# Performance work log

Hardware: AMD Instinct MI355X
Metric: run time of the kernel (lower is better)

The kernel has to match this reference:

```python
import jax, jax.numpy as jnp
import numpy as np

INPUT_SIZE = 512
HIDDEN_SIZE = 512
BATCH = 64
SEQ = 1024

def _xavier(key, shape):
    fan_in, fan_out = shape
    limit = float(np.sqrt(6.0 / (fan_in + fan_out)))
    return jax.random.uniform(key, shape, jnp.float32, -limit, limit)

def setup_inputs() -> dict:
    key = jax.random.key(0)
    ks = jax.random.split(key, 9)
    x = jax.random.normal(ks[0], (BATCH, SEQ, INPUT_SIZE), jnp.float32)
    # Concatenate the 4 input-hidden and 4 hidden-hidden weights (i,f,g,o order)
    W_i = jnp.concatenate([_xavier(ks[1 + j], (INPUT_SIZE, HIDDEN_SIZE)) for j in range(4)], axis=1)  # [I, 4H]
    W_h = jnp.concatenate([_xavier(ks[5 + j], (HIDDEN_SIZE, HIDDEN_SIZE)) for j in range(4)], axis=1)  # [H, 4H]
    b = jnp.zeros((4 * HIDDEN_SIZE,), jnp.float32)  # b_ii+b_hi etc. are both zero-init; combined bias
    return {"x": x, "W_i": W_i, "W_h": W_h, "b": b}

def reference(x, W_i, W_h, b):
    H = W_h.shape[0]
    B = x.shape[0]
    # Precompute all input projections in one big GEMM: [B, S, 4H]
    x_proj = jnp.einsum('bsi,ig->bsg', x, W_i) + b

    def step(carry, xp_t):
        h, c = carry
        gates = xp_t + h @ W_h  # [B, 4H]
        i_t = jax.nn.sigmoid(gates[:, 0*H:1*H])
        f_t = jax.nn.sigmoid(gates[:, 1*H:2*H])
        g_t = jnp.tanh(gates[:, 2*H:3*H])
        o_t = jax.nn.sigmoid(gates[:, 3*H:4*H])
        c = f_t * c + i_t * g_t
        h = o_t * jnp.tanh(c)
        return (h, c), None

    h0 = jnp.zeros((B, H), x.dtype)
    c0 = jnp.zeros((B, H), x.dtype)
    (h_t, c_t), _ = jax.lax.scan(step, (h0, c0), jnp.swapaxes(x_proj, 0, 1))
    return (h_t, c_t)
```

## Files before the change

### kernel.cpp

```cpp
#include <hip/hip_runtime.h>
#include <hip/hip_bf16.h>
#include <hip/hip_cooperative_groups.h>

namespace cg = cooperative_groups;

typedef unsigned short ushort_t;
typedef unsigned int uint32;
typedef __attribute__((ext_vector_type(8))) __bf16 bf16x8;
typedef __attribute__((ext_vector_type(4))) float f32x4;
typedef __attribute__((ext_vector_type(4))) unsigned int u32x4;

#define SEQ_LEN 1024
#define NWG 64
#define NTHR 256

#define XPACK_BYTES (64ull << 20)
#define WPACK_BYTES (4ull << 20)
#define HB_OFF  (XPACK_BYTES + WPACK_BYTES)
#define CNT_OFF (HB_OFF + (128ull << 10))
#define WS_NEED (CNT_OFF + (64ull << 10))

__device__ __forceinline__ ushort_t f2bf(float f) {
  unsigned u = __builtin_bit_cast(unsigned, f);
  unsigned r = (u + 0x7fffu + ((u >> 16) & 1u)) >> 16;
  return (ushort_t)r;
}
__device__ __forceinline__ float sigm(float x) {
  float e = __expf(-x);
  return __builtin_amdgcn_rcpf(1.f + e);
}
__device__ __forceinline__ float tanh_fast(float x) {
  float a = fabsf(x);
  float e = __expf(-2.f * a);
  float r = (1.f - e) * __builtin_amdgcn_rcpf(1.f + e);
  return copysignf(r, x);
}

__global__ void zero_mem_kernel(u32x4* p) {
  int i = blockIdx.x * blockDim.x + threadIdx.x;
  u32x4 z = {0u, 0u, 0u, 0u};
  p[i] = z;
}

__global__ void pack_x_kernel(const float* __restrict__ x, u32x4* __restrict__ xp) {
  unsigned u = blockIdx.x * blockDim.x + threadIdx.x;
  int hi = u & 3;
  int kk = (u >> 2) & 15;
  int t  = (u >> 6) & 1023;
  int b  = u >> 16;
  const float* src = x + (((size_t)b * SEQ_LEN + t) * 512 + (kk << 5) + (hi << 3));
  f32x4 f0 = *(const f32x4*)(src);
  f32x4 f1 = *(const f32x4*)(src + 4);
  u32x4 o;
  o[0] = f2bf(f0[0]) | ((uint32)f2bf(f0[1]) << 16);
  o[1] = f2bf(f0[2]) | ((uint32)f2bf(f0[3]) << 16);
  o[2] = f2bf(f1[0]) | ((uint32)f2bf(f1[1]) << 16);
  o[3] = f2bf(f1[2]) | ((uint32)f2bf(f1[3]) << 16);
  xp[(size_t)((t * 16 + kk) * 64 + b) * 4 + hi] = o;
}

__global__ void pack_w_kernel(const float* __restrict__ Wi, const float* __restrict__ Wh,
                              ushort_t* __restrict__ wp) {
  unsigned e = blockIdx.x * blockDim.x + threadIdx.x;
  int k = e >> 11;
  int col = e & 2047;
  float v = (k < 512) ? Wi[(size_t)k * 2048 + col] : Wh[(size_t)(k - 512) * 2048 + col];
  int wg  = (col & 511) >> 3;
  int tau = (col >> 2) & 1;
  int hcl = col & 3;
  int gate = col >> 9;
  int p = (hcl << 2) | gate;
  int kk = k >> 5;
  int hi = (k >> 3) & 3;
  int r = k & 7;
  int lane = (hi << 4) | p;
  wp[(size_t)wg * 32768 + (size_t)(((kk * 2) + tau) * 64 + lane) * 8 + r] = f2bf(v);
}

template<bool FAST>
__global__ void __launch_bounds__(NTHR, 1)
lstm_coop(const float* __restrict__ x, const float* __restrict__ Wi,
          const float* __restrict__ Wh, const float* __restrict__ bias,
          const u32x4* __restrict__ xpack, const u32x4* __restrict__ wpack,
          ushort_t* hbuf, uint32* flags, float* out)
{
  __shared__ u32x4 lA[4096];
  const int tid  = threadIdx.x;
  const int wg   = blockIdx.x;
  const int lane = tid & 63;
  const int wv   = tid >> 6;
  const int hi2  = lane >> 4;
  const int lo   = lane & 15;
  const int b    = (wv << 4) | lo;

  if (FAST) {
    const u32x4* wsrc = wpack + (size_t)wg * 2048 * 2;
    for (int i = tid; i < 4096; i += NTHR) lA[i] = wsrc[i];
  } else {
    for (int uu = tid; uu < 4096; uu += NTHR) {
      int ln = uu & 63, tau = (uu >> 6) & 1, kk = uu >> 7;
      int uhi = ln >> 4, p = ln & 15;
      int gate = p & 3, hcl = p >> 2;
      int col = gate * 512 + (wg << 3) + tau * 4 + hcl;
      ushort_t tmp[8];
#pragma unroll
      for (int r = 0; r < 8; ++r) {
        int k = (kk << 5) + (uhi << 3) + r;
        float f = (k < 512) ? Wi[(size_t)k * 2048 + col] : Wh[(size_t)(k - 512) * 2048 + col];
        tmp[r] = f2bf(f);
      }
      u32x4 v;
      v[0] = tmp[0] | ((uint32)tmp[1] << 16);
      v[1] = tmp[2] | ((uint32)tmp[3] << 16);
      v[2] = tmp[4] | ((uint32)tmp[5] << 16);
      v[3] = tmp[6] | ((uint32)tmp[7] << 16);
      lA[uu] = v;
    }
  }
  __syncthreads();

  const int kh0 = (wg << 3) | hi2;
  const int kh1 = kh0 + 4;
  const float b00 = bias[0 * 512 + kh0], b01 = bias[1 * 512 + kh0];
  const float b02 = bias[2 * 512 + kh0], b03 = bias[3 * 512 + kh0];
  const float b10 = bias[0 * 512 + kh1], b11 = bias[1 * 512 + kh1];
  const float b12 = bias[2 * 512 + kh1], b13 = bias[3 * 512 + kh1];

  const int hoff0 = (((kh0 >> 5) * 256 + b * 4 + ((kh0 >> 3) & 3)) << 3) + (kh0 & 7);
  const int hoff1 = hoff0 + 4;

  bf16x8 whA[16], whB[16];
#pragma unroll
  for (int kk = 0; kk < 16; ++kk) {
    whA[kk] = __builtin_bit_cast(bf16x8, lA[((16 + kk) * 2 + 0) * 64 + lane]);
    whB[kk] = __builtin_bit_cast(bf16x8, lA[((16 + kk) * 2 + 1) * 64 + lane]);
  }

  float c0 = 0.f, c1 = 0.f, hn0 = 0.f, hn1 = 0.f;
  cg::grid_group grid = cg::this_grid();

  for (int t = 0; t < SEQ_LEN; ++t) {
    f32x4 ax0 = {b00, b01, b02, b03};
    f32x4 ax1 = {b10, b11, b12, b13};
    if (FAST) {
      const u32x4* xb = xpack + (size_t)t * 4096 + b * 4 + hi2;
#pragma unroll
      for (int kk = 0; kk < 16; ++kk) {
        bf16x8 xv = __builtin_bit_cast(bf16x8, xb[kk * 256]);
        bf16x8 a0 = __builtin_bit_cast(bf16x8, lA[(kk * 2 + 0) * 64 + lane]);
        bf16x8 a1 = __builtin_bit_cast(bf16x8, lA[(kk * 2 + 1) * 64 + lane]);
        ax0 = __builtin_amdgcn_mfma_f32_16x16x32_bf16(a0, xv, ax0, 0, 0, 0);
        ax1 = __builtin_amdgcn_mfma_f32_16x16x32_bf16(a1, xv, ax1, 0, 0, 0);
      }
    } else {
      const float* xr = x + ((size_t)b * SEQ_LEN + t) * 512 + (hi2 << 3);
#pragma unroll
      for (int kk = 0; kk < 16; ++kk) {
        f32x4 f0 = *(const f32x4*)(xr + (kk << 5));
        f32x4 f1 = *(const f32x4*)(xr + (kk << 5) + 4);
        u32x4 v;
        v[0] = f2bf(f0[0]) | ((uint32)f2bf(f0[1]) << 16);
        v[1] = f2bf(f0[2]) | ((uint32)f2bf(f0[3]) << 16);
        v[2] = f2bf(f1[0]) | ((uint32)f2bf(f1[1]) << 16);
        v[3] = f2bf(f1[2]) | ((uint32)f2bf(f1[3]) << 16);
        bf16x8 xv = __builtin_bit_cast(bf16x8, v);
        bf16x8 a0 = __builtin_bit_cast(bf16x8, lA[(kk * 2 + 0) * 64 + lane]);
        bf16x8 a1 = __builtin_bit_cast(bf16x8, lA[(kk * 2 + 1) * 64 + lane]);
        ax0 = __builtin_amdgcn_mfma_f32_16x16x32_bf16(a0, xv, ax0, 0, 0, 0);
        ax1 = __builtin_amdgcn_mfma_f32_16x16x32_bf16(a1, xv, ax1, 0, 0, 0);
      }
    }

    if (FAST) {
      if (t > 0) {
        const u32x4* fa = (const u32x4*)flags + lane;
        const uint32 tt = (uint32)t;
        while (true) {
          u32x4 v;
          asm volatile("global_load_dwordx4 %0, %1, off sc0 sc1\n\ts_waitcnt vmcnt(0)"
                       : "=v"(v) : "v"(fa) : "memory");
          bool ok = (v[0] >= tt) & (v[1] >= tt) & (v[2] >= tt) & (v[3] >= tt);
          if (__all(ok)) break;
        }
      }
    }

    const u32x4* hr = (const u32x4*)hbuf + (size_t)(t & 1) * 4096 + b * 4 + hi2;
    u32x4 hreg[16];
    if (FAST) {
#pragma unroll
      for (int kk = 0; kk < 16; ++kk)
        asm volatile("global_load_dwordx4 %0, %1, off sc0 sc1"
                     : "=v"(hreg[kk]) : "v"(hr + kk * 256) : "memory");
      asm volatile("s_waitcnt vmcnt(0)" ::: "memory");
      __builtin_amdgcn_sched_barrier(0);
    } else {
#pragma unroll
      for (int kk = 0; kk < 16; ++kk) hreg[kk] = hr[kk * 256];
    }

    f32x4 ah0 = {0.f, 0.f, 0.f, 0.f};
    f32x4 ah1 = {0.f, 0.f, 0.f, 0.f};
#pragma unroll
    for (int kk = 0; kk < 16; ++kk) {
      bf16x8 hv = __builtin_bit_cast(bf16x8, hreg[kk]);
      ah0 = __builtin_amdgcn_mfma_f32_16x16x32_bf16(whA[kk], hv, ah0, 0, 0, 0);
      ah1 = __builtin_amdgcn_mfma_f32_16x16x32_bf16(whB[kk], hv, ah1, 0, 0, 0);
    }

    {
      float gi = ax0[0] + ah0[0], gf = ax0[1] + ah0[1];
      float gg = ax0[2] + ah0[2], go = ax0[3] + ah0[3];
      float it = sigm(gi), ft = sigm(gf), ot = sigm(go), gt = tanh_fast(gg);
      c0 = ft * c0 + it * gt;
      hn0 = ot * tanh_fast(c0);
    }
    {
      float gi = ax1[0] + ah1[0], gf = ax1[1] + ah1[1];
      float gg = ax1[2] + ah1[2], go = ax1[3] + ah1[3];
      float it = sigm(gi), ft = sigm(gf), ot = sigm(go), gt = tanh_fast(gg);
      c1 = ft * c1 + it * gt;
      hn1 = ot * tanh_fast(c1);
    }

    if (t < SEQ_LEN - 1) {
      ushort_t* hw = hbuf + (size_t)((t + 1) & 1) * 32768;
      if (FAST) {
        uint32 v0 = f2bf(hn0), v1 = f2bf(hn1);
        asm volatile("global_store_short %0, %1, off sc0 sc1"
                     :: "v"(hw + hoff0), "v"(v0) : "memory");
        asm volatile("global_store_short %0, %1, off sc0 sc1"
                     :: "v"(hw + hoff1), "v"(v1) : "memory");
        asm volatile("s_waitcnt vmcnt(0)" ::: "memory");
        __builtin_amdgcn_sched_barrier(0);
        if (lane == 0) {
          uint32* fp = flags + (wg << 2) + wv;
          uint32 val = (uint32)(t + 1);
          asm volatile("global_store_dword %0, %1, off sc0 sc1"
                       :: "v"(fp), "v"(val) : "memory");
        }
      } else {
        hw[hoff0] = f2bf(hn0);
        hw[hoff1] = f2bf(hn1);
        __threadfence();
        grid.sync();
        __threadfence();
      }
    } else if (!FAST) {
      __threadfence();
      grid.sync();
    }
  }

  out[(size_t)b * 512 + kh0] = hn0;
  out[(size_t)b * 512 + kh1] = hn1;
  out[32768 + (size_t)b * 512 + kh0] = c0;
  out[32768 + (size_t)b * 512 + kh1] = c1;
}

extern "C" void kernel_launch(void* const* d_in, const int* in_sizes, int n_in,
                              void* d_out, int out_size, void* d_ws, size_t ws_size,
                              hipStream_t stream) {
  const float* x    = (const float*)d_in[0];
  const float* Wi   = (const float*)d_in[1];
  const float* Wh   = (const float*)d_in[2];
  const float* bias = (const float*)d_in[3];
  float* out = (float*)d_out;

  bool fast = (d_ws != nullptr) && (ws_size >= WS_NEED);

  if (fast) {
    const u32x4* xpack = (const u32x4*)d_ws;
    const u32x4* wpack = (const u32x4*)((char*)d_ws + XPACK_BYTES);
    ushort_t* hbuf = (ushort_t*)((char*)d_ws + HB_OFF);
    uint32* flags = (uint32*)((char*)d_ws + CNT_OFF);

    zero_mem_kernel<<<48, 256, 0, stream>>>((u32x4*)((char*)d_ws + HB_OFF));
    pack_x_kernel<<<16384, 256, 0, stream>>>(x, (u32x4*)d_ws);
    pack_w_kernel<<<8192, 256, 0, stream>>>(Wi, Wh, (ushort_t*)((char*)d_ws + XPACK_BYTES));

    void* args[] = {(void*)&x, (void*)&Wi, (void*)&Wh, (void*)&bias,
                    (void*)&xpack, (void*)&wpack, (void*)&hbuf, (void*)&flags, (void*)&out};
    void (*kfn)(const float*, const float*, const float*, const float*,
                const u32x4*, const u32x4*, ushort_t*, uint32*, float*) = lstm_coop<true>;
    hipLaunchCooperativeKernel(reinterpret_cast<void*>(kfn), dim3(NWG), dim3(NTHR),
                               args, 0, stream);
  } else {
    ushort_t* hbuf = (ushort_t*)d_out;
    uint32* flags = (uint32*)d_out;
    const u32x4* xpack = (const u32x4*)x;
    const u32x4* wpack = (const u32x4*)Wi;

    zero_mem_kernel<<<16, 256, 0, stream>>>((u32x4*)d_out);

    void* args[] = {(void*)&x, (void*)&Wi, (void*)&Wh, (void*)&bias,
                    (void*)&xpack, (void*)&wpack, (void*)&hbuf, (void*)&flags, (void*)&out};
    void (*kfn)(const float*, const float*, const float*, const float*,
                const u32x4*, const u32x4*, ushort_t*, uint32*, float*) = lstm_coop<false>;
    hipLaunchCooperativeKernel(reinterpret_cast<void*>(kfn), dim3(NWG), dim3(NTHR),
                               args, 0, stream);
  }
}
```

Before: 3.231 ms.

## Tag hidden-state words with timestep to replace flag polling with data polling

Each bf16 hidden value is now stored as a 32-bit word whose high half carries the timestep, so consumers poll the hidden-state buffer itself and proceed once every loaded word has the expected tag. This removes the separate flag array, the store-wait before publishing a flag, and the extra round trip of flag-then-data loads on each step. In exchange every step loads twice as many bytes of hidden state and repacks them before the MFMAs. The fast path also switches from a cooperative launch to a normal launch, which relies on all 64 workgroups being co-resident.

```diff
diff --git a/kernel.cpp b/kernel.cpp
--- a/kernel.cpp
+++ b/kernel.cpp
@@ -17,8 +17,7 @@
 #define XPACK_BYTES (64ull << 20)
 #define WPACK_BYTES (4ull << 20)
 #define HB_OFF  (XPACK_BYTES + WPACK_BYTES)
-#define CNT_OFF (HB_OFF + (128ull << 10))
-#define WS_NEED (CNT_OFF + (64ull << 10))
+#define WS_NEED (HB_OFF + (256ull << 10))
 
 __device__ __forceinline__ ushort_t f2bf(float f) {
   unsigned u = __builtin_bit_cast(unsigned, f);
@@ -35,6 +34,7 @@
   float r = (1.f - e) * __builtin_amdgcn_rcpf(1.f + e);
   return copysignf(r, x);
 }
+__device__ __forceinline__ uint32 umin2(uint32 a, uint32 b) { return a < b ? a : b; }
 
 __global__ void zero_mem_kernel(u32x4* p) {
   int i = blockIdx.x * blockDim.x + threadIdx.x;
@@ -82,7 +82,7 @@
 lstm_coop(const float* __restrict__ x, const float* __restrict__ Wi,
           const float* __restrict__ Wh, const float* __restrict__ bias,
           const u32x4* __restrict__ xpack, const u32x4* __restrict__ wpack,
-          ushort_t* hbuf, uint32* flags, float* out)
+          uint32* hbuf32, ushort_t* hbuf16, float* out)
 {
   __shared__ u32x4 lA[4096];
   const int tid  = threadIdx.x;
@@ -93,7 +93,7 @@
   const int lo   = lane & 15;
   const int b    = (wv << 4) | lo;
 
-  if (FAST) {
+  if constexpr (FAST) {
     const u32x4* wsrc = wpack + (size_t)wg * 2048 * 2;
     for (int i = tid; i < 4096; i += NTHR) lA[i] = wsrc[i];
   } else {
@@ -137,12 +137,11 @@
   }
 
   float c0 = 0.f, c1 = 0.f, hn0 = 0.f, hn1 = 0.f;
-  cg::grid_group grid = cg::this_grid();
 
   for (int t = 0; t < SEQ_LEN; ++t) {
     f32x4 ax0 = {b00, b01, b02, b03};
     f32x4 ax1 = {b10, b11, b12, b13};
-    if (FAST) {
+    if constexpr (FAST) {
       const u32x4* xb = xpack + (size_t)t * 4096 + b * 4 + hi2;
 #pragma unroll
       for (int kk = 0; kk < 16; ++kk) {
@@ -171,41 +170,52 @@
       }
     }
 
-    if (FAST) {
-      if (t > 0) {
-        const u32x4* fa = (const u32x4*)flags + lane;
-        const uint32 tt = (uint32)t;
-        while (true) {
-          u32x4 v;
-          asm volatile("global_load_dwordx4 %0, %1, off sc0 sc1\n\ts_waitcnt vmcnt(0)"
-                       : "=v"(v) : "v"(fa) : "memory");
-          bool ok = (v[0] >= tt) & (v[1] >= tt) & (v[2] >= tt) & (v[3] >= tt);
-          if (__all(ok)) break;
-        }
-      }
-    }
-
-    const u32x4* hr = (const u32x4*)hbuf + (size_t)(t & 1) * 4096 + b * 4 + hi2;
-    u32x4 hreg[16];
-    if (FAST) {
-#pragma unroll
-      for (int kk = 0; kk < 16; ++kk)
-        asm volatile("global_load_dwordx4 %0, %1, off sc0 sc1"
-                     : "=v"(hreg[kk]) : "v"(hr + kk * 256) : "memory");
-      asm volatile("s_waitcnt vmcnt(0)" ::: "memory");
-      __builtin_amdgcn_sched_barrier(0);
-    } else {
-#pragma unroll
-      for (int kk = 0; kk < 16; ++kk) hreg[kk] = hr[kk * 256];
-    }
-
     f32x4 ah0 = {0.f, 0.f, 0.f, 0.f};
     f32x4 ah1 = {0.f, 0.f, 0.f, 0.f};
-#pragma unroll
-    for (int kk = 0; kk < 16; ++kk) {
-      bf16x8 hv = __builtin_bit_cast(bf16x8, hreg[kk]);
-      ah0 = __builtin_amdgcn_mfma_f32_16x16x32_bf16(whA[kk], hv, ah0, 0, 0, 0);
-      ah1 = __builtin_amdgcn_mfma_f32_16x16x32_bf16(whB[kk], hv, ah1, 0, 0, 0);
+
+    if constexpr (FAST) {
+      const u32x4* hr = (const u32x4*)hbuf32 + (size_t)(t & 1) * 8192
+                        + ((size_t)b * 4 + hi2) * 2;
+      const uint32 thr = (uint32)t << 16;
+      u32x4 hreg[32];
+      while (true) {
+#pragma unroll
+        for (int kk = 0; kk < 16; ++kk) {
+          asm volatile("global_load_dwordx4 %0, %1, off sc0 sc1"
+                       : "=v"(hreg[2 * kk]) : "v"(hr + kk * 512) : "memory");
+          asm volatile("global_load_dwordx4 %0, %1, off sc0 sc1"
+                       : "=v"(hreg[2 * kk + 1]) : "v"(hr + kk * 512 + 1) : "memory");
+        }
+        asm volatile("s_waitcnt vmcnt(0)" ::: "memory");
+        __builtin_amdgcn_sched_barrier(0);
+        uint32 mn = 0xFFFFFFFFu;
+#pragma unroll
+        for (int i = 0; i < 32; ++i) {
+          u32x4 v = hreg[i];
+          mn = umin2(mn, umin2(umin2(v[0], v[1]), umin2(v[2], v[3])));
+        }
+        if (__all(mn >= thr)) break;
+      }
+#pragma unroll
+      for (int kk = 0; kk < 16; ++kk) {
+        u32x4 lo4 = hreg[2 * kk], hi4 = hreg[2 * kk + 1];
+        u32x4 p;
+        p[0] = (lo4[0] & 0xFFFFu) | (lo4[1] << 16);
+        p[1] = (lo4[2] & 0xFFFFu) | (lo4[3] << 16);
+        p[2] = (hi4[0] & 0xFFFFu) | (hi4[1] << 16);
+        p[3] = (hi4[2] & 0xFFFFu) | (hi4[3] << 16);
+        bf16x8 hv = __builtin_bit_cast(bf16x8, p);
+        ah0 = __builtin_amdgcn_mfma_f32_16x16x32_bf16(whA[kk], hv, ah0, 0, 0, 0);
+        ah1 = __builtin_amdgcn_mfma_f32_16x16x32_bf16(whB[kk], hv, ah1, 0, 0, 0);
+      }
+    } else {
+      const u32x4* hr = (const u32x4*)hbuf16 + (size_t)(t & 1) * 4096 + b * 4 + hi2;
+#pragma unroll
+      for (int kk = 0; kk < 16; ++kk) {
+        bf16x8 hv = __builtin_bit_cast(bf16x8, hr[kk * 256]);
+        ah0 = __builtin_amdgcn_mfma_f32_16x16x32_bf16(whA[kk], hv, ah0, 0, 0, 0);
+        ah1 = __builtin_amdgcn_mfma_f32_16x16x32_bf16(whB[kk], hv, ah1, 0, 0, 0);
+      }
     }
 
     {
@@ -224,31 +234,28 @@
     }
 
     if (t < SEQ_LEN - 1) {
-      ushort_t* hw = hbuf + (size_t)((t + 1) & 1) * 32768;
-      if (FAST) {
-        uint32 v0 = f2bf(hn0), v1 = f2bf(hn1);
-        asm volatile("global_store_short %0, %1, off sc0 sc1"
-                     :: "v"(hw + hoff0), "v"(v0) : "memory");
-        asm volatile("global_store_short %0, %1, off sc0 sc1"
-                     :: "v"(hw + hoff1), "v"(v1) : "memory");
-        asm volatile("s_waitcnt vmcnt(0)" ::: "memory");
-        __builtin_amdgcn_sched_barrier(0);
-        if (lane == 0) {
-          uint32* fp = flags + (wg << 2) + wv;
-          uint32 val = (uint32)(t + 1);
-          asm volatile("global_store_dword %0, %1, off sc0 sc1"
-                       :: "v"(fp), "v"(val) : "memory");
-        }
+      if constexpr (FAST) {
+        uint32* hw = hbuf32 + (size_t)((t + 1) & 1) * 32768;
+        uint32 tag = (uint32)(t + 1) << 16;
+        uint32 w0 = tag | f2bf(hn0);
+        uint32 w1 = tag | f2bf(hn1);
+        asm volatile("global_store_dword %0, %1, off sc0 sc1"
+                     :: "v"(hw + hoff0), "v"(w0) : "memory");
+        asm volatile("global_store_dword %0, %1, off sc0 sc1"
+                     :: "v"(hw + hoff1), "v"(w1) : "memory");
       } else {
+        ushort_t* hw = hbuf16 + (size_t)((t + 1) & 1) * 32768;
         hw[hoff0] = f2bf(hn0);
         hw[hoff1] = f2bf(hn1);
         __threadfence();
-        grid.sync();
+        cg::this_grid().sync();
         __threadfence();
       }
-    } else if (!FAST) {
-      __threadfence();
-      grid.sync();
+    } else {
+      if constexpr (!FAST) {
+        __threadfence();
+        cg::this_grid().sync();
+      }
     }
   }
 
@@ -272,31 +279,27 @@
   if (fast) {
     const u32x4* xpack = (const u32x4*)d_ws;
     const u32x4* wpack = (const u32x4*)((char*)d_ws + XPACK_BYTES);
-    ushort_t* hbuf = (ushort_t*)((char*)d_ws + HB_OFF);
-    uint32* flags = (uint32*)((char*)d_ws + CNT_OFF);
-
-    zero_mem_kernel<<<48, 256, 0, stream>>>((u32x4*)((char*)d_ws + HB_OFF));
+    uint32* hbuf32 = (uint32*)((char*)d_ws + HB_OFF);
+    ushort_t* hbuf16 = (ushort_t*)d_out;
+
+    zero_mem_kernel<<<64, 256, 0, stream>>>((u32x4*)((char*)d_ws + HB_OFF));
     pack_x_kernel<<<16384, 256, 0, stream>>>(x, (u32x4*)d_ws);
     pack_w_kernel<<<8192, 256, 0, stream>>>(Wi, Wh, (ushort_t*)((char*)d_ws + XPACK_BYTES));
 
-    void* args[] = {(void*)&x, (void*)&Wi, (void*)&Wh, (void*)&bias,
-                    (void*)&xpack, (void*)&wpack, (void*)&hbuf, (void*)&flags, (void*)&out};
-    void (*kfn)(const float*, const float*, const float*, const float*,
-                const u32x4*, const u32x4*, ushort_t*, uint32*, float*) = lstm_coop<true>;
-    hipLaunchCooperativeKernel(reinterpret_cast<void*>(kfn), dim3(NWG), dim3(NTHR),
-                               args, 0, stream);
+    lstm_coop<true><<<dim3(NWG), dim3(NTHR), 0, stream>>>(
+        x, Wi, Wh, bias, xpack, wpack, hbuf32, hbuf16, out);
   } else {
-    ushort_t* hbuf = (ushort_t*)d_out;
-    uint32* flags = (uint32*)d_out;
+    uint32* hbuf32 = (uint32*)d_out;
+    ushort_t* hbuf16 = (ushort_t*)d_out;
     const u32x4* xpack = (const u32x4*)x;
     const u32x4* wpack = (const u32x4*)Wi;
 
     zero_mem_kernel<<<16, 256, 0, stream>>>((u32x4*)d_out);
 
     void* args[] = {(void*)&x, (void*)&Wi, (void*)&Wh, (void*)&bias,
-                    (void*)&xpack, (void*)&wpack, (void*)&hbuf, (void*)&flags, (void*)&out};
+                    (void*)&xpack, (void*)&wpack, (void*)&hbuf32, (void*)&hbuf16, (void*)&out};
     void (*kfn)(const float*, const float*, const float*, const float*,
-                const u32x4*, const u32x4*, ushort_t*, uint32*, float*) = lstm_coop<false>;
+                const u32x4*, const u32x4*, uint32*, ushort_t*, float*) = lstm_coop<false>;
     hipLaunchCooperativeKernel(reinterpret_cast<void*>(kfn), dim3(NWG), dim3(NTHR),
                                args, 0, stream);
   }
```

New measurement: 8.557 ms. +164.9%, slower.

## Drop x pre-pack, keep weights in registers, use per-step h buffers

Applied to the files above, without the earlier changes.

Removes the separate pack_x kernel so the recurrent kernel reads fp32 x directly and converts it to bf16 on the fly. This avoids a full 256MB read and 64MB write pass before the recurrence starts. Both the input and hidden weight tiles now live in VGPRs instead of LDS. The ping-pong h buffer becomes one buffer slot per timestep (64MB), which removes write-after-read hazards. The flag poll loads one dword per lane instead of a dwordx4, and the fast path uses a normal launch instead of a cooperative one. The trade-offs are higher register pressure, more global x traffic inside the serial loop, and relying on all 64 blocks being co-resident without a cooperative-launch guarantee.

```diff
diff --git a/kernel.cpp b/kernel.cpp
--- a/kernel.cpp
+++ b/kernel.cpp
@@ -14,11 +14,10 @@
 #define NWG 64
 #define NTHR 256
 
-#define XPACK_BYTES (64ull << 20)
 #define WPACK_BYTES (4ull << 20)
-#define HB_OFF  (XPACK_BYTES + WPACK_BYTES)
-#define CNT_OFF (HB_OFF + (128ull << 10))
-#define WS_NEED (CNT_OFF + (64ull << 10))
+#define HB_OFF  WPACK_BYTES
+#define FLG_OFF (HB_OFF + (64ull << 20))
+#define WS_NEED (FLG_OFF + (4ull << 10))
 
 __device__ __forceinline__ ushort_t f2bf(float f) {
   unsigned u = __builtin_bit_cast(unsigned, f);
@@ -40,23 +39,6 @@
   int i = blockIdx.x * blockDim.x + threadIdx.x;
   u32x4 z = {0u, 0u, 0u, 0u};
   p[i] = z;
-}
-
-__global__ void pack_x_kernel(const float* __restrict__ x, u32x4* __restrict__ xp) {
-  unsigned u = blockIdx.x * blockDim.x + threadIdx.x;
-  int hi = u & 3;
-  int kk = (u >> 2) & 15;
-  int t  = (u >> 6) & 1023;
-  int b  = u >> 16;
-  const float* src = x + (((size_t)b * SEQ_LEN + t) * 512 + (kk << 5) + (hi << 3));
-  f32x4 f0 = *(const f32x4*)(src);
-  f32x4 f1 = *(const f32x4*)(src + 4);
-  u32x4 o;
-  o[0] = f2bf(f0[0]) | ((uint32)f2bf(f0[1]) << 16);
-  o[1] = f2bf(f0[2]) | ((uint32)f2bf(f0[3]) << 16);
-  o[2] = f2bf(f1[0]) | ((uint32)f2bf(f1[1]) << 16);
-  o[3] = f2bf(f1[2]) | ((uint32)f2bf(f1[3]) << 16);
-  xp[(size_t)((t * 16 + kk) * 64 + b) * 4 + hi] = o;
 }
 
 __global__ void pack_w_kernel(const float* __restrict__ Wi, const float* __restrict__ Wh,
@@ -81,10 +63,9 @@
 __global__ void __launch_bounds__(NTHR, 1)
 lstm_coop(const float* __restrict__ x, const float* __restrict__ Wi,
           const float* __restrict__ Wh, const float* __restrict__ bias,
-          const u32x4* __restrict__ xpack, const u32x4* __restrict__ wpack,
-          ushort_t* hbuf, uint32* flags, float* out)
+          const u32x4* __restrict__ wpack, ushort_t* hbuf16, uint32* flags, float* out)
 {
-  __shared__ u32x4 lA[4096];
+  __shared__ u32x4 lA[FAST ? 1 : 4096];
   const int tid  = threadIdx.x;
   const int wg   = blockIdx.x;
   const int lane = tid & 63;
@@ -93,9 +74,17 @@
   const int lo   = lane & 15;
   const int b    = (wv << 4) | lo;
 
-  if (FAST) {
-    const u32x4* wsrc = wpack + (size_t)wg * 2048 * 2;
-    for (int i = tid; i < 4096; i += NTHR) lA[i] = wsrc[i];
+  bf16x8 wxA[16], wxB[16], whA[16], whB[16];
+
+  if constexpr (FAST) {
+    const u32x4* wsrc = wpack + (size_t)wg * 4096;
+#pragma unroll
+    for (int kk = 0; kk < 16; ++kk) {
+      wxA[kk] = __builtin_bit_cast(bf16x8, wsrc[(kk * 2 + 0) * 64 + lane]);
+      wxB[kk] = __builtin_bit_cast(bf16x8, wsrc[(kk * 2 + 1) * 64 + lane]);
+      whA[kk] = __builtin_bit_cast(bf16x8, wsrc[((16 + kk) * 2 + 0) * 64 + lane]);
+      whB[kk] = __builtin_bit_cast(bf16x8, wsrc[((16 + kk) * 2 + 1) * 64 + lane]);
+    }
   } else {
     for (int uu = tid; uu < 4096; uu += NTHR) {
       int ln = uu & 63, tau = (uu >> 6) & 1, kk = uu >> 7;
@@ -116,8 +105,13 @@
       v[3] = tmp[6] | ((uint32)tmp[7] << 16);
       lA[uu] = v;
     }
+    __syncthreads();
+#pragma unroll
+    for (int kk = 0; kk < 16; ++kk) {
+      whA[kk] = __builtin_bit_cast(bf16x8, lA[((16 + kk) * 2 + 0) * 64 + lane]);
+      whB[kk] = __builtin_bit_cast(bf16x8, lA[((16 + kk) * 2 + 1) * 64 + lane]);
+    }
   }
-  __syncthreads();
 
   const int kh0 = (wg << 3) | hi2;
   const int kh1 = kh0 + 4;
@@ -129,30 +123,12 @@
   const int hoff0 = (((kh0 >> 5) * 256 + b * 4 + ((kh0 >> 3) & 3)) << 3) + (kh0 & 7);
   const int hoff1 = hoff0 + 4;
 
-  bf16x8 whA[16], whB[16];
-#pragma unroll
-  for (int kk = 0; kk < 16; ++kk) {
-    whA[kk] = __builtin_bit_cast(bf16x8, lA[((16 + kk) * 2 + 0) * 64 + lane]);
-    whB[kk] = __builtin_bit_cast(bf16x8, lA[((16 + kk) * 2 + 1) * 64 + lane]);
-  }
-
   float c0 = 0.f, c1 = 0.f, hn0 = 0.f, hn1 = 0.f;
-  cg::grid_group grid = cg::this_grid();
 
   for (int t = 0; t < SEQ_LEN; ++t) {
     f32x4 ax0 = {b00, b01, b02, b03};
     f32x4 ax1 = {b10, b11, b12, b13};
-    if (FAST) {
-      const u32x4* xb = xpack + (size_t)t * 4096 + b * 4 + hi2;
-#pragma unroll
-      for (int kk = 0; kk < 16; ++kk) {
-        bf16x8 xv = __builtin_bit_cast(bf16x8, xb[kk * 256]);
-        bf16x8 a0 = __builtin_bit_cast(bf16x8, lA[(kk * 2 + 0) * 64 + lane]);
-        bf16x8 a1 = __builtin_bit_cast(bf16x8, lA[(kk * 2 + 1) * 64 + lane]);
-        ax0 = __builtin_amdgcn_mfma_f32_16x16x32_bf16(a0, xv, ax0, 0, 0, 0);
-        ax1 = __builtin_amdgcn_mfma_f32_16x16x32_bf16(a1, xv, ax1, 0, 0, 0);
-      }
-    } else {
+    {
       const float* xr = x + ((size_t)b * SEQ_LEN + t) * 512 + (hi2 << 3);
 #pragma unroll
       for (int kk = 0; kk < 16; ++kk) {
@@ -164,48 +140,51 @@
         v[2] = f2bf(f1[0]) | ((uint32)f2bf(f1[1]) << 16);
         v[3] = f2bf(f1[2]) | ((uint32)f2bf(f1[3]) << 16);
         bf16x8 xv = __builtin_bit_cast(bf16x8, v);
-        bf16x8 a0 = __builtin_bit_cast(bf16x8, lA[(kk * 2 + 0) * 64 + lane]);
-        bf16x8 a1 = __builtin_bit_cast(bf16x8, lA[(kk * 2 + 1) * 64 + lane]);
-        ax0 = __builtin_amdgcn_mfma_f32_16x16x32_bf16(a0, xv, ax0, 0, 0, 0);
-        ax1 = __builtin_amdgcn_mfma_f32_16x16x32_bf16(a1, xv, ax1, 0, 0, 0);
-      }
-    }
-
-    if (FAST) {
+        if constexpr (FAST) {
+          ax0 = __builtin_amdgcn_mfma_f32_16x16x32_bf16(wxA[kk], xv, ax0, 0, 0, 0);
+          ax1 = __builtin_amdgcn_mfma_f32_16x16x32_bf16(wxB[kk], xv, ax1, 0, 0, 0);
+        } else {
+          bf16x8 a0 = __builtin_bit_cast(bf16x8, lA[(kk * 2 + 0) * 64 + lane]);
+          bf16x8 a1 = __builtin_bit_cast(bf16x8, lA[(kk * 2 + 1) * 64 + lane]);
+          ax0 = __builtin_amdgcn_mfma_f32_16x16x32_bf16(a0, xv, ax0, 0, 0, 0);
+          ax1 = __builtin_amdgcn_mfma_f32_16x16x32_bf16(a1, xv, ax1, 0, 0, 0);
+        }
+      }
+    }
+
+    f32x4 ah0 = {0.f, 0.f, 0.f, 0.f};
+    f32x4 ah1 = {0.f, 0.f, 0.f, 0.f};
+
+    if constexpr (FAST) {
       if (t > 0) {
-        const u32x4* fa = (const u32x4*)flags + lane;
+        const uint32* fa = flags + (lane << 2) + wv;
         const uint32 tt = (uint32)t;
         while (true) {
-          u32x4 v;
-          asm volatile("global_load_dwordx4 %0, %1, off sc0 sc1\n\ts_waitcnt vmcnt(0)"
+          uint32 v;
+          asm volatile("global_load_dword %0, %1, off sc0 sc1\n\ts_waitcnt vmcnt(0)"
                        : "=v"(v) : "v"(fa) : "memory");
-          bool ok = (v[0] >= tt) & (v[1] >= tt) & (v[2] >= tt) & (v[3] >= tt);
-          if (__all(ok)) break;
+          if (__all(v >= tt)) break;
         }
-      }
-    }
-
-    const u32x4* hr = (const u32x4*)hbuf + (size_t)(t & 1) * 4096 + b * 4 + hi2;
-    u32x4 hreg[16];
-    if (FAST) {
-#pragma unroll
-      for (int kk = 0; kk < 16; ++kk)
-        asm volatile("global_load_dwordx4 %0, %1, off sc0 sc1"
-                     : "=v"(hreg[kk]) : "v"(hr + kk * 256) : "memory");
-      asm volatile("s_waitcnt vmcnt(0)" ::: "memory");
-      __builtin_amdgcn_sched_barrier(0);
+        __builtin_amdgcn_sched_barrier(0);
+      }
+      const u32x4* hr = (const u32x4*)(hbuf16 + (size_t)t * 32768) + b * 4 + hi2;
+      u32x4 hreg[16];
+#pragma unroll
+      for (int kk = 0; kk < 16; ++kk) hreg[kk] = hr[kk * 256];
+#pragma unroll
+      for (int kk = 0; kk < 16; ++kk) {
+        bf16x8 hv = __builtin_bit_cast(bf16x8, hreg[kk]);
+        ah0 = __builtin_amdgcn_mfma_f32_16x16x32_bf16(whA[kk], hv, ah0, 0, 0, 0);
+        ah1 = __builtin_amdgcn_mfma_f32_16x16x32_bf16(whB[kk], hv, ah1, 0, 0, 0);
+      }
     } else {
-#pragma unroll
-      for (int kk = 0; kk < 16; ++kk) hreg[kk] = hr[kk * 256];
-    }
-
-    f32x4 ah0 = {0.f, 0.f, 0.f, 0.f};
-    f32x4 ah1 = {0.f, 0.f, 0.f, 0.f};
-#pragma unroll
-    for (int kk = 0; kk < 16; ++kk) {
-      bf16x8 hv = __builtin_bit_cast(bf16x8, hreg[kk]);
-      ah0 = __builtin_amdgcn_mfma_f32_16x16x32_bf16(whA[kk], hv, ah0, 0, 0, 0);
-      ah1 = __builtin_amdgcn_mfma_f32_16x16x32_bf16(whB[kk], hv, ah1, 0, 0, 0);
+      const u32x4* hr = (const u32x4*)hbuf16 + (size_t)(t & 1) * 4096 + b * 4 + hi2;
+#pragma unroll
+      for (int kk = 0; kk < 16; ++kk) {
+        bf16x8 hv = __builtin_bit_cast(bf16x8, hr[kk * 256]);
+        ah0 = __builtin_amdgcn_mfma_f32_16x16x32_bf16(whA[kk], hv, ah0, 0, 0, 0);
+        ah1 = __builtin_amdgcn_mfma_f32_16x16x32_bf16(whB[kk], hv, ah1, 0, 0, 0);
+      }
     }
 
     {
@@ -224,8 +203,8 @@
     }
 
     if (t < SEQ_LEN - 1) {
-      ushort_t* hw = hbuf + (size_t)((t + 1) & 1) * 32768;
-      if (FAST) {
+      if constexpr (FAST) {
+        ushort_t* hw = hbuf16 + (size_t)(t + 1) * 32768;
         uint32 v0 = f2bf(hn0), v1 = f2bf(hn1);
         asm volatile("global_store_short %0, %1, off sc0 sc1"
                      :: "v"(hw + hoff0), "v"(v0) : "memory");
@@ -240,15 +219,18 @@
                        :: "v"(fp), "v"(val) : "memory");
         }
       } else {
+        ushort_t* hw = hbuf16 + (size_t)((t + 1) & 1) * 32768;
         hw[hoff0] = f2bf(hn0);
         hw[hoff1] = f2bf(hn1);
         __threadfence();
-        grid.sync();
+        cg::this_grid().sync();
         __threadfence();
       }
-    } else if (!FAST) {
-      __threadfence();
-      grid.sync();
+    } else {
+      if constexpr (!FAST) {
+        __threadfence();
+        cg::this_grid().sync();
+      }
     }
   }
 
@@ -270,33 +252,27 @@
   bool fast = (d_ws != nullptr) && (ws_size >= WS_NEED);
 
   if (fast) {
-    const u32x4* xpack = (const u32x4*)d_ws;
-    const u32x4* wpack = (const u32x4*)((char*)d_ws + XPACK_BYTES);
-    ushort_t* hbuf = (ushort_t*)((char*)d_ws + HB_OFF);
-    uint32* flags = (uint32*)((char*)d_ws + CNT_OFF);
-
-    zero_mem_kernel<<<48, 256, 0, stream>>>((u32x4*)((char*)d_ws + HB_OFF));
-    pack_x_kernel<<<16384, 256, 0, stream>>>(x, (u32x4*)d_ws);
-    pack_w_kernel<<<8192, 256, 0, stream>>>(Wi, Wh, (ushort_t*)((char*)d_ws + XPACK_BYTES));
+    const u32x4* wpack = (const u32x4*)d_ws;
+    ushort_t* hbuf16 = (ushort_t*)((char*)d_ws + HB_OFF);
+    uint32* flags    = (uint32*)((char*)d_ws + FLG_OFF);
+
+    zero_mem_kernel<<<16, 256, 0, stream>>>((u32x4*)((char*)d_ws + HB_OFF));
+    zero_mem_kernel<<<1, 256, 0, stream>>>((u32x4*)((char*)d_ws + FLG_OFF));
+    pack_w_kernel<<<8192, 256, 0, stream>>>(Wi, Wh, (ushort_t*)d_ws);
+
+    lstm_coop<true><<<dim3(NWG), dim3(NTHR), 0, stream>>>(
+        x, Wi, Wh, bias, wpack, hbuf16, flags, out);
+  } else {
+    ushort_t* hbuf16 = (ushort_t*)d_out;
+    uint32* flags = (uint32*)d_out;
+    const u32x4* wpack = (const u32x4*)Wi;
+
+    zero_mem_kernel<<<16, 256, 0, stream>>>((u32x4*)d_out);
 
     void* args[] = {(void*)&x, (void*)&Wi, (void*)&Wh, (void*)&bias,
-                    (void*)&xpack, (void*)&wpack, (void*)&hbuf, (void*)&flags, (void*)&out};
+                    (void*)&wpack, (void*)&hbuf16, (void*)&flags, (void*)&out};
     void (*kfn)(const float*, const float*, const float*, const float*,
-                const u32x4*, const u32x4*, ushort_t*, uint32*, float*) = lstm_coop<true>;
-    hipLaunchCooperativeKernel(reinterpret_cast<void*>(kfn), dim3(NWG), dim3(NTHR),
-                               args, 0, stream);
-  } else {
-    ushort_t* hbuf = (ushort_t*)d_out;
-    uint32* flags = (uint32*)d_out;
-    const u32x4* xpack = (const u32x4*)x;
-    const u32x4* wpack = (const u32x4*)Wi;
-
-    zero_mem_kernel<<<16, 256, 0, stream>>>((u32x4*)d_out);
-
-    void* args[] = {(void*)&x, (void*)&Wi, (void*)&Wh, (void*)&bias,
-                    (void*)&xpack, (void*)&wpack, (void*)&hbuf, (void*)&flags, (void*)&out};
-    void (*kfn)(const float*, const float*, const float*, const float*,
-                const u32x4*, const u32x4*, ushort_t*, uint32*, float*) = lstm_coop<false>;
+                const u32x4*, ushort_t*, uint32*, float*) = lstm_coop<false>;
     hipLaunchCooperativeKernel(reinterpret_cast<void*>(kfn), dim3(NWG), dim3(NTHR),
                                args, 0, stream);
   }
```

Measured after the change: 9.070 ms. 2.81x slower.

## Halve workgroup count so each handles 16 hidden units, skip h-GEMM at t=0

Applied to the files above, without the earlier changes.

Splits the LSTM over 32 workgroups instead of 64, each owning 16 hidden units (four MFMA tiles per wave). The W_h slices now stay in LDS rather than registers. The flag array shrinks to one dword per wave and workgroup, polled with a single dword load per lane. Packed x and h are laid out so each lane reads contiguous 16-byte chunks. The recurrent GEMM is skipped at t=0, and the fast path uses a plain launch instead of a cooperative one. Fewer workgroups means fewer participants in the per-step synchronisation, at the cost of twice the MFMA work per workgroup on the serial critical path.

```diff
diff --git a/kernel.cpp b/kernel.cpp
--- a/kernel.cpp
+++ b/kernel.cpp
@@ -11,14 +11,14 @@
 typedef __attribute__((ext_vector_type(4))) unsigned int u32x4;
 
 #define SEQ_LEN 1024
-#define NWG 64
+#define NWG 32
 #define NTHR 256
 
 #define XPACK_BYTES (64ull << 20)
 #define WPACK_BYTES (4ull << 20)
 #define HB_OFF  (XPACK_BYTES + WPACK_BYTES)
-#define CNT_OFF (HB_OFF + (128ull << 10))
-#define WS_NEED (CNT_OFF + (64ull << 10))
+#define FLG_OFF (HB_OFF + (128ull << 10))
+#define WS_NEED (FLG_OFF + (4ull << 10))
 
 __device__ __forceinline__ ushort_t f2bf(float f) {
   unsigned u = __builtin_bit_cast(unsigned, f);
@@ -44,11 +44,14 @@
 
 __global__ void pack_x_kernel(const float* __restrict__ x, u32x4* __restrict__ xp) {
   unsigned u = blockIdx.x * blockDim.x + threadIdx.x;
-  int hi = u & 3;
-  int kk = (u >> 2) & 15;
-  int t  = (u >> 6) & 1023;
-  int b  = u >> 16;
-  const float* src = x + (((size_t)b * SEQ_LEN + t) * 512 + (kk << 5) + (hi << 3));
+  int lane = u & 63;
+  int kk   = (u >> 6) & 15;
+  int bq   = (u >> 10) & 3;
+  int t    = u >> 12;
+  int hi2 = lane >> 4, lo = lane & 15;
+  int b  = bq * 16 + lo;
+  int k0 = kk * 32 + hi2 * 8;
+  const float* src = x + ((size_t)b * SEQ_LEN + t) * 512 + k0;
   f32x4 f0 = *(const f32x4*)(src);
   f32x4 f1 = *(const f32x4*)(src + 4);
   u32x4 o;
@@ -56,7 +59,7 @@
   o[1] = f2bf(f0[2]) | ((uint32)f2bf(f0[3]) << 16);
   o[2] = f2bf(f1[0]) | ((uint32)f2bf(f1[1]) << 16);
   o[3] = f2bf(f1[2]) | ((uint32)f2bf(f1[3]) << 16);
-  xp[(size_t)((t * 16 + kk) * 64 + b) * 4 + hi] = o;
+  xp[u] = o;
 }
 
 __global__ void pack_w_kernel(const float* __restrict__ Wi, const float* __restrict__ Wh,
@@ -65,8 +68,8 @@
   int k = e >> 11;
   int col = e & 2047;
   float v = (k < 512) ? Wi[(size_t)k * 2048 + col] : Wh[(size_t)(k - 512) * 2048 + col];
-  int wg  = (col & 511) >> 3;
-  int tau = (col >> 2) & 1;
+  int wg  = (col & 511) >> 4;
+  int tau = (col >> 2) & 3;
   int hcl = col & 3;
   int gate = col >> 9;
   int p = (hcl << 2) | gate;
@@ -74,7 +77,7 @@
   int hi = (k >> 3) & 3;
   int r = k & 7;
   int lane = (hi << 4) | p;
-  wp[(size_t)wg * 32768 + (size_t)(((kk * 2) + tau) * 64 + lane) * 8 + r] = f2bf(v);
+  wp[(size_t)wg * 65536 + (size_t)((kk * 4 + tau) * 64 + lane) * 8 + r] = f2bf(v);
 }
 
 template<bool FAST>
@@ -84,7 +87,7 @@
           const u32x4* __restrict__ xpack, const u32x4* __restrict__ wpack,
           ushort_t* hbuf, uint32* flags, float* out)
 {
-  __shared__ u32x4 lA[4096];
+  __shared__ u32x4 lA[8192];
   const int tid  = threadIdx.x;
   const int wg   = blockIdx.x;
   const int lane = tid & 63;
@@ -93,15 +96,15 @@
   const int lo   = lane & 15;
   const int b    = (wv << 4) | lo;
 
-  if (FAST) {
-    const u32x4* wsrc = wpack + (size_t)wg * 2048 * 2;
-    for (int i = tid; i < 4096; i += NTHR) lA[i] = wsrc[i];
+  if constexpr (FAST) {
+    const u32x4* wsrc = wpack + (size_t)wg * 8192;
+    for (int i = tid; i < 8192; i += NTHR) lA[i] = wsrc[i];
   } else {
-    for (int uu = tid; uu < 4096; uu += NTHR) {
-      int ln = uu & 63, tau = (uu >> 6) & 1, kk = uu >> 7;
+    for (int uu = tid; uu < 8192; uu += NTHR) {
+      int ln = uu & 63, tau = (uu >> 6) & 3, kk = uu >> 8;
       int uhi = ln >> 4, p = ln & 15;
       int gate = p & 3, hcl = p >> 2;
-      int col = gate * 512 + (wg << 3) + tau * 4 + hcl;
+      int col = gate * 512 + (wg << 4) + tau * 4 + hcl;
       ushort_t tmp[8];
 #pragma unroll
       for (int r = 0; r < 8; ++r) {
@@ -119,143 +122,136 @@
   }
   __syncthreads();
 
-  const int kh0 = (wg << 3) | hi2;
-  const int kh1 = kh0 + 4;
-  const float b00 = bias[0 * 512 + kh0], b01 = bias[1 * 512 + kh0];
-  const float b02 = bias[2 * 512 + kh0], b03 = bias[3 * 512 + kh0];
-  const float b10 = bias[0 * 512 + kh1], b11 = bias[1 * 512 + kh1];
-  const float b12 = bias[2 * 512 + kh1], b13 = bias[3 * 512 + kh1];
-
-  const int hoff0 = (((kh0 >> 5) * 256 + b * 4 + ((kh0 >> 3) & 3)) << 3) + (kh0 & 7);
-  const int hoff1 = hoff0 + 4;
-
-  bf16x8 whA[16], whB[16];
-#pragma unroll
-  for (int kk = 0; kk < 16; ++kk) {
-    whA[kk] = __builtin_bit_cast(bf16x8, lA[((16 + kk) * 2 + 0) * 64 + lane]);
-    whB[kk] = __builtin_bit_cast(bf16x8, lA[((16 + kk) * 2 + 1) * 64 + lane]);
-  }
-
-  float c0 = 0.f, c1 = 0.f, hn0 = 0.f, hn1 = 0.f;
-  cg::grid_group grid = cg::this_grid();
+  int kh[4], uoff[4];
+  float bia[4][4];
+#pragma unroll
+  for (int tau = 0; tau < 4; ++tau) {
+    int k = (wg << 4) + tau * 4 + hi2;
+    kh[tau] = k;
+    uoff[tau] = ((wv * 1024 + (k >> 5) * 64 + ((k >> 3) & 3) * 16 + lo) << 3) + (k & 7);
+#pragma unroll
+    for (int g = 0; g < 4; ++g) bia[tau][g] = bias[g * 512 + k];
+  }
+
+  float c[4] = {0.f, 0.f, 0.f, 0.f};
+  float hn[4] = {0.f, 0.f, 0.f, 0.f};
 
   for (int t = 0; t < SEQ_LEN; ++t) {
-    f32x4 ax0 = {b00, b01, b02, b03};
-    f32x4 ax1 = {b10, b11, b12, b13};
-    if (FAST) {
-      const u32x4* xb = xpack + (size_t)t * 4096 + b * 4 + hi2;
-#pragma unroll
-      for (int kk = 0; kk < 16; ++kk) {
-        bf16x8 xv = __builtin_bit_cast(bf16x8, xb[kk * 256]);
-        bf16x8 a0 = __builtin_bit_cast(bf16x8, lA[(kk * 2 + 0) * 64 + lane]);
-        bf16x8 a1 = __builtin_bit_cast(bf16x8, lA[(kk * 2 + 1) * 64 + lane]);
-        ax0 = __builtin_amdgcn_mfma_f32_16x16x32_bf16(a0, xv, ax0, 0, 0, 0);
-        ax1 = __builtin_amdgcn_mfma_f32_16x16x32_bf16(a1, xv, ax1, 0, 0, 0);
-      }
-    } else {
-      const float* xr = x + ((size_t)b * SEQ_LEN + t) * 512 + (hi2 << 3);
-#pragma unroll
-      for (int kk = 0; kk < 16; ++kk) {
-        f32x4 f0 = *(const f32x4*)(xr + (kk << 5));
-        f32x4 f1 = *(const f32x4*)(xr + (kk << 5) + 4);
+    f32x4 ax0 = {bia[0][0], bia[0][1], bia[0][2], bia[0][3]};
+    f32x4 ax1 = {bia[1][0], bia[1][1], bia[1][2], bia[1][3]};
+    f32x4 ax2 = {bia[2][0], bia[2][1], bia[2][2], bia[2][3]};
+    f32x4 ax3 = {bia[3][0], bia[3][1], bia[3][2], bia[3][3]};
+#pragma unroll
+    for (int kk = 0; kk < 16; ++kk) {
+      bf16x8 xv;
+      if constexpr (FAST) {
+        xv = __builtin_bit_cast(bf16x8, xpack[(size_t)t * 4096 + wv * 1024 + kk * 64 + lane]);
+      } else {
+        const float* xr = x + ((size_t)b * SEQ_LEN + t) * 512 + (kk << 5) + (hi2 << 3);
+        f32x4 f0 = *(const f32x4*)(xr);
+        f32x4 f1 = *(const f32x4*)(xr + 4);
         u32x4 v;
         v[0] = f2bf(f0[0]) | ((uint32)f2bf(f0[1]) << 16);
         v[1] = f2bf(f0[2]) | ((uint32)f2bf(f0[3]) << 16);
         v[2] = f2bf(f1[0]) | ((uint32)f2bf(f1[1]) << 16);
         v[3] = f2bf(f1[2]) | ((uint32)f2bf(f1[3]) << 16);
-        bf16x8 xv = __builtin_bit_cast(bf16x8, v);
-        bf16x8 a0 = __builtin_bit_cast(bf16x8, lA[(kk * 2 + 0) * 64 + lane]);
-        bf16x8 a1 = __builtin_bit_cast(bf16x8, lA[(kk * 2 + 1) * 64 + lane]);
-        ax0 = __builtin_amdgcn_mfma_f32_16x16x32_bf16(a0, xv, ax0, 0, 0, 0);
-        ax1 = __builtin_amdgcn_mfma_f32_16x16x32_bf16(a1, xv, ax1, 0, 0, 0);
-      }
-    }
-
-    if (FAST) {
-      if (t > 0) {
-        const u32x4* fa = (const u32x4*)flags + lane;
+        xv = __builtin_bit_cast(bf16x8, v);
+      }
+      ax0 = __builtin_amdgcn_mfma_f32_16x16x32_bf16(
+              __builtin_bit_cast(bf16x8, lA[(kk * 4 + 0) * 64 + lane]), xv, ax0, 0, 0, 0);
+      ax1 = __builtin_amdgcn_mfma_f32_16x16x32_bf16(
+              __builtin_bit_cast(bf16x8, lA[(kk * 4 + 1) * 64 + lane]), xv, ax1, 0, 0, 0);
+      ax2 = __builtin_amdgcn_mfma_f32_16x16x32_bf16(
+              __builtin_bit_cast(bf16x8, lA[(kk * 4 + 2) * 64 + lane]), xv, ax2, 0, 0, 0);
+      ax3 = __builtin_amdgcn_mfma_f32_16x16x32_bf16(
+              __builtin_bit_cast(bf16x8, lA[(kk * 4 + 3) * 64 + lane]), xv, ax3, 0, 0, 0);
+    }
+
+    if (t > 0) {
+      if constexpr (FAST) {
+        const uint32* fa = flags + wv * 32 + (lane & 31);
         const uint32 tt = (uint32)t;
         while (true) {
-          u32x4 v;
-          asm volatile("global_load_dwordx4 %0, %1, off sc0 sc1\n\ts_waitcnt vmcnt(0)"
+          uint32 v;
+          asm volatile("global_load_dword %0, %1, off sc0 sc1\n\ts_waitcnt vmcnt(0)"
                        : "=v"(v) : "v"(fa) : "memory");
-          bool ok = (v[0] >= tt) & (v[1] >= tt) & (v[2] >= tt) & (v[3] >= tt);
-          if (__all(ok)) break;
+          if (__all(v >= tt)) break;
         }
-      }
-    }
-
-    const u32x4* hr = (const u32x4*)hbuf + (size_t)(t & 1) * 4096 + b * 4 + hi2;
-    u32x4 hreg[16];
-    if (FAST) {
-#pragma unroll
-      for (int kk = 0; kk < 16; ++kk)
-        asm volatile("global_load_dwordx4 %0, %1, off sc0 sc1"
-                     : "=v"(hreg[kk]) : "v"(hr + kk * 256) : "memory");
-      asm volatile("s_waitcnt vmcnt(0)" ::: "memory");
-      __builtin_amdgcn_sched_barrier(0);
-    } else {
-#pragma unroll
-      for (int kk = 0; kk < 16; ++kk) hreg[kk] = hr[kk * 256];
-    }
-
-    f32x4 ah0 = {0.f, 0.f, 0.f, 0.f};
-    f32x4 ah1 = {0.f, 0.f, 0.f, 0.f};
-#pragma unroll
-    for (int kk = 0; kk < 16; ++kk) {
-      bf16x8 hv = __builtin_bit_cast(bf16x8, hreg[kk]);
-      ah0 = __builtin_amdgcn_mfma_f32_16x16x32_bf16(whA[kk], hv, ah0, 0, 0, 0);
-      ah1 = __builtin_amdgcn_mfma_f32_16x16x32_bf16(whB[kk], hv, ah1, 0, 0, 0);
-    }
-
-    {
-      float gi = ax0[0] + ah0[0], gf = ax0[1] + ah0[1];
-      float gg = ax0[2] + ah0[2], go = ax0[3] + ah0[3];
+        __builtin_amdgcn_sched_barrier(0);
+      }
+      const u32x4* hr = (const u32x4*)(hbuf + (size_t)(t & 1) * 32768) + wv * 1024 + lane;
+      u32x4 hreg[16];
+      if constexpr (FAST) {
+#pragma unroll
+        for (int kk = 0; kk < 16; ++kk)
+          asm volatile("global_load_dwordx4 %0, %1, off sc0 sc1"
+                       : "=v"(hreg[kk]) : "v"(hr + kk * 64) : "memory");
+        asm volatile("s_waitcnt vmcnt(0)" ::: "memory");
+        __builtin_amdgcn_sched_barrier(0);
+      } else {
+#pragma unroll
+        for (int kk = 0; kk < 16; ++kk) hreg[kk] = hr[kk * 64];
+      }
+#pragma unroll
+      for (int kk = 0; kk < 16; ++kk) {
+        bf16x8 hv = __builtin_bit_cast(bf16x8, hreg[kk]);
+        ax0 = __builtin_amdgcn_mfma_f32_16x16x32_bf16(
+                __builtin_bit_cast(bf16x8, lA[((16 + kk) * 4 + 0) * 64 + lane]), hv, ax0, 0, 0, 0);
+        ax1 = __builtin_amdgcn_mfma_f32_16x16x32_bf16(
+                __builtin_bit_cast(bf16x8, lA[((16 + kk) * 4 + 1) * 64 + lane]), hv, ax1, 0, 0, 0);
+        ax2 = __builtin_amdgcn_mfma_f32_16x16x32_bf16(
+                __builtin_bit_cast(bf16x8, lA[((16 + kk) * 4 + 2) * 64 + lane]), hv, ax2, 0, 0, 0);
+        ax3 = __builtin_amdgcn_mfma_f32_16x16x32_bf16(
+                __builtin_bit_cast(bf16x8, lA[((16 + kk) * 4 + 3) * 64 + lane]), hv, ax3, 0, 0, 0);
+      }
+    }
+
+    f32x4 axv[4] = {ax0, ax1, ax2, ax3};
+#pragma unroll
+    for (int tau = 0; tau < 4; ++tau) {
+      float gi = axv[tau][0], gf = axv[tau][1], gg = axv[tau][2], go = axv[tau][3];
       float it = sigm(gi), ft = sigm(gf), ot = sigm(go), gt = tanh_fast(gg);
-      c0 = ft * c0 + it * gt;
-      hn0 = ot * tanh_fast(c0);
-    }
-    {
-      float gi = ax1[0] + ah1[0], gf = ax1[1] + ah1[1];
-      float gg = ax1[2] + ah1[2], go = ax1[3] + ah1[3];
-      float it = sigm(gi), ft = sigm(gf), ot = sigm(go), gt = tanh_fast(gg);
-      c1 = ft * c1 + it * gt;
-      hn1 = ot * tanh_fast(c1);
+      c[tau] = ft * c[tau] + it * gt;
+      hn[tau] = ot * tanh_fast(c[tau]);
     }
 
     if (t < SEQ_LEN - 1) {
       ushort_t* hw = hbuf + (size_t)((t + 1) & 1) * 32768;
-      if (FAST) {
-        uint32 v0 = f2bf(hn0), v1 = f2bf(hn1);
-        asm volatile("global_store_short %0, %1, off sc0 sc1"
-                     :: "v"(hw + hoff0), "v"(v0) : "memory");
-        asm volatile("global_store_short %0, %1, off sc0 sc1"
-                     :: "v"(hw + hoff1), "v"(v1) : "memory");
+      if constexpr (FAST) {
+#pragma unroll
+        for (int tau = 0; tau < 4; ++tau) {
+          uint32 v = f2bf(hn[tau]);
+          asm volatile("global_store_short %0, %1, off sc0 sc1"
+                       :: "v"(hw + uoff[tau]), "v"(v) : "memory");
+        }
         asm volatile("s_waitcnt vmcnt(0)" ::: "memory");
         __builtin_amdgcn_sched_barrier(0);
         if (lane == 0) {
-          uint32* fp = flags + (wg << 2) + wv;
+          uint32* fp = flags + wv * 32 + wg;
           uint32 val = (uint32)(t + 1);
           asm volatile("global_store_dword %0, %1, off sc0 sc1"
                        :: "v"(fp), "v"(val) : "memory");
         }
       } else {
-        hw[hoff0] = f2bf(hn0);
-        hw[hoff1] = f2bf(hn1);
+#pragma unroll
+        for (int tau = 0; tau < 4; ++tau) hw[uoff[tau]] = f2bf(hn[tau]);
         __threadfence();
-        grid.sync();
+        cg::this_grid().sync();
         __threadfence();
       }
-    } else if (!FAST) {
-      __threadfence();
-      grid.sync();
-    }
-  }
-
-  out[(size_t)b * 512 + kh0] = hn0;
-  out[(size_t)b * 512 + kh1] = hn1;
-  out[32768 + (size_t)b * 512 + kh0] = c0;
-  out[32768 + (size_t)b * 512 + kh1] = c1;
+    } else {
+      if constexpr (!FAST) {
+        __threadfence();
+        cg::this_grid().sync();
+      }
+    }
+  }
+
+#pragma unroll
+  for (int tau = 0; tau < 4; ++tau) {
+    out[(size_t)b * 512 + kh[tau]] = hn[tau];
+    out[32768 + (size_t)b * 512 + kh[tau]] = c[tau];
+  }
 }
 
 extern "C" void kernel_launch(void* const* d_in, const int* in_sizes, int n_in,
@@ -273,25 +269,19 @@
     const u32x4* xpack = (const u32x4*)d_ws;
     const u32x4* wpack = (const u32x4*)((char*)d_ws + XPACK_BYTES);
     ushort_t* hbuf = (ushort_t*)((char*)d_ws + HB_OFF);
-    uint32* flags = (uint32*)((char*)d_ws + CNT_OFF);
-
-    zero_mem_kernel<<<48, 256, 0, stream>>>((u32x4*)((char*)d_ws + HB_OFF));
+    uint32* flags  = (uint32*)((char*)d_ws + FLG_OFF);
+
+    zero_mem_kernel<<<1, 32, 0, stream>>>((u32x4*)((char*)d_ws + FLG_OFF));
     pack_x_kernel<<<16384, 256, 0, stream>>>(x, (u32x4*)d_ws);
     pack_w_kernel<<<8192, 256, 0, stream>>>(Wi, Wh, (ushort_t*)((char*)d_ws + XPACK_BYTES));
 
-    void* args[] = {(void*)&x, (void*)&Wi, (void*)&Wh, (void*)&bias,
-                    (void*)&xpack, (void*)&wpack, (void*)&hbuf, (void*)&flags, (void*)&out};
-    void (*kfn)(const float*, const float*, const float*, const float*,
-                const u32x4*, const u32x4*, ushort_t*, uint32*, float*) = lstm_coop<true>;
-    hipLaunchCooperativeKernel(reinterpret_cast<void*>(kfn), dim3(NWG), dim3(NTHR),
-                               args, 0, stream);
+    lstm_coop<true><<<dim3(NWG), dim3(NTHR), 0, stream>>>(
+        x, Wi, Wh, bias, xpack, wpack, hbuf, flags, out);
   } else {
     ushort_t* hbuf = (ushort_t*)d_out;
     uint32* flags = (uint32*)d_out;
     const u32x4* xpack = (const u32x4*)x;
     const u32x4* wpack = (const u32x4*)Wi;
-
-    zero_mem_kernel<<<16, 256, 0, stream>>>((u32x4*)d_out);
 
     void* args[] = {(void*)&x, (void*)&Wi, (void*)&Wh, (void*)&bias,
                     (void*)&xpack, (void*)&wpack, (void*)&hbuf, (void*)&flags, (void*)&out};
```

After: 3.883 ms. 1.2x slower.
